# Optimization experiments

Hardware: AMD Instinct MI355X
Metric: run time of the kernel (lower is better)

Reference implementation:

```python
import jax, jax.numpy as jnp
import numpy as np

PAD_IDX = 0
K = 5
TEMPERATURE = 1.0
BATCH = 256
VOCAB = 50257


def setup_inputs() -> dict:
    key = jax.random.key(0)
    k1, k2, k3, k4, k5 = jax.random.split(key, 5)
    draft_tokens = jax.random.randint(k1, (BATCH, K), 0, VOCAB)
    # valid-ish log-probabilities (negative values)
    draft_log_probs = -jax.random.uniform(k2, (BATCH, K), minval=0.05, maxval=8.0, dtype=jnp.float32)
    target_logits = jax.random.normal(k3, (BATCH, K, VOCAB), dtype=jnp.float32)
    random_vals = jax.random.uniform(k4, (BATCH, K), dtype=jnp.float32)
    uniform_sample = jax.random.uniform(k5, (BATCH,), dtype=jnp.float32)
    return {
        "draft_tokens": draft_tokens,
        "draft_log_probs": draft_log_probs,
        "target_logits": target_logits,
        "random_vals": random_vals,
        "uniform_sample": uniform_sample,
    }


def reference(draft_tokens, draft_log_probs, target_logits, random_vals, uniform_sample):
    B, k = draft_tokens.shape
    # --- accept/reject scan ---
    tlp = jax.nn.log_softmax(target_logits / TEMPERATURE, axis=-1)          # [B,k,V]
    tlp_draft = jnp.take_along_axis(tlp, draft_tokens[..., None], axis=2)[..., 0]  # [B,k]
    accept_probs = jnp.minimum(jnp.exp(tlp_draft - draft_log_probs), 1.0)
    accepted_mask = random_vals < accept_probs
    rejected_sent = jnp.concatenate(
        [~accepted_mask, jnp.ones((B, 1), dtype=bool)], axis=1)              # [B,k+1]
    first_reject = jnp.argmax(rejected_sent, axis=1)                         # [B]
    n_accepted = first_reject
    # fixed-width (k) accepted_tokens, PAD-filled past n_accepted (jit-friendly
    # variant of torch's dynamic max_accepted truncation; same valid entries)
    pos = jnp.arange(k)[None, :]
    accepted_tokens = jnp.where(pos < n_accepted[:, None], draft_tokens, PAD_IDX)
    # --- vectorized fallback sampling at first reject position ---
    rp = jnp.minimum(first_reject, k - 1)                                    # clamp for gather
    sel_logits = jnp.take_along_axis(target_logits, rp[:, None, None], axis=1)[:, 0, :]  # [B,V]
    target_probs = jax.nn.softmax(sel_logits / TEMPERATURE, axis=-1)
    dlp_sel = jnp.take_along_axis(draft_log_probs, rp[:, None], axis=1)      # [B,1]
    # torch builds a constant vector exp(dlp) over the whole vocab
    draft_probs = jnp.exp(dlp_sel)                                           # [B,1] broadcasts
    adjusted = jnp.clip(target_probs - draft_probs, 0.0)
    s = adjusted.sum(axis=-1, keepdims=True)
    probs = jnp.where(s > 0, adjusted / jnp.where(s > 0, s, 1.0), target_probs)  # [B,V]
    # multinomial(probs, 1) via inverse CDF with provided uniform sample
    cdf = jnp.cumsum(probs, axis=-1)
    thresh = uniform_sample[:, None] * cdf[:, -1:]
    sampled = jnp.argmax(cdf >= thresh, axis=-1)                             # [B]
    final_tokens = jnp.where(first_reject < k, sampled, PAD_IDX)
    return accepted_tokens, n_accepted, final_tokens
```

## Files before the change

kernel.cpp:

```cpp
#include <hip/hip_runtime.h>
#include <math.h>
#include <stdint.h>

#define VOCAB 50257
#define KD 5
#define NBATCH 256
#define NSPLIT 8
#define SEG ((VOCAB + NSPLIT - 1) / NSPLIT)
#define NT1 256
#define NT2 1024
#define NW2 (NT2 / 64)
#define NTILES ((VOCAB + NT2 - 1) / NT2)

__global__ __launch_bounds__(NT1) void zsum_row0_kernel(
    const float* __restrict__ logits, double* __restrict__ part)
{
    const int bid = blockIdx.x;
    const int b   = bid / NSPLIT;
    const int seg = bid % NSPLIT;
    const int tid = threadIdx.x;
    const int lane = tid & 63, wv = tid >> 6;

    const float* row = logits + (size_t)b * KD * (size_t)VOCAB;
    int s0 = seg * SEG;
    int s1 = s0 + SEG; if (s1 > VOCAB) s1 = VOCAB;
    const float* p = row + s0;
    int n = s1 - s0;

    int head = (int)((4u - ((((uintptr_t)p) >> 2) & 3u)) & 3u);
    if (head > n) head = n;
    double local = 0.0;
    if (tid < head) local += (double)expf(p[tid]);
    int nvec = (n - head) >> 2;
    const float4* p4 = (const float4*)(p + head);
    for (int i = tid; i < nvec; i += NT1) {
        float4 x = p4[i];
        local += (double)expf(x.x) + (double)expf(x.y)
               + (double)expf(x.z) + (double)expf(x.w);
    }
    int ts = head + (nvec << 2);
    int tc = n - ts;
    if (tid < tc) local += (double)expf(p[ts + tid]);

    for (int off = 32; off; off >>= 1) local += __shfl_down(local, off, 64);
    __shared__ double sw[NT1 / 64];
    if (lane == 0) sw[wv] = local;
    __syncthreads();
    if (tid == 0) {
        double Z = 0.0;
        for (int w = 0; w < NT1 / 64; ++w) Z += sw[w];
        part[bid] = Z;
    }
}

__global__ __launch_bounds__(NT2) void decide_sample_kernel(
    const int* __restrict__ dtok,
    const float* __restrict__ dlp,
    const float* __restrict__ logits,
    const float* __restrict__ rnd,
    const float* __restrict__ usmp,
    const double* __restrict__ part,
    int* __restrict__ out)
{
    const int b    = blockIdx.x;
    const int tid  = threadIdx.x;
    const int lane = tid & 63;
    const int wv   = tid >> 6;

    __shared__ double s_w[NW2];
    __shared__ double s_tileA[NTILES];
    __shared__ double s_tileR[NTILES];
    __shared__ double s_dbc[2];
    __shared__ int    s_ibc[2];
    __shared__ int    s_found;

    double Zsel  = 0.0;
    int    n_acc = KD;
    for (int r = 0; r < KD; ++r) {
        const float* row = logits + ((size_t)b * KD + r) * (size_t)VOCAB;
        if (r > 0) {
            int head = (int)((4u - ((((uintptr_t)row) >> 2) & 3u)) & 3u);
            double local = 0.0;
            if (tid < head) local += (double)expf(row[tid]);
            int nvec = (VOCAB - head) >> 2;
            const float4* row4 = (const float4*)(row + head);
            for (int i = tid; i < nvec; i += NT2) {
                float4 x = row4[i];
                local += (double)expf(x.x) + (double)expf(x.y)
                       + (double)expf(x.z) + (double)expf(x.w);
            }
            int ts = head + (nvec << 2);
            int tc = VOCAB - ts;
            if (tid < tc) local += (double)expf(row[ts + tid]);
            for (int off = 32; off; off >>= 1) local += __shfl_down(local, off, 64);
            if (lane == 0) s_w[wv] = local;
            __syncthreads();
            if (tid == 0) {
                double Z = 0.0;
                for (int w = 0; w < NW2; ++w) Z += s_w[w];
                s_dbc[0] = Z;
            }
            __syncthreads();
        } else {
            if (wv == 0) {
                double v = (lane < NSPLIT) ? part[b * NSPLIT + lane] : 0.0;
                for (int off = 4; off; off >>= 1) v += __shfl_down(v, off, 64);
                if (lane == 0) s_dbc[0] = v;
            }
            __syncthreads();
        }
        if (tid == 0) {
            double Z   = s_dbc[0];
            int    tok = dtok[b * KD + r];
            double tlp = (double)row[tok] - log(Z);
            double ap  = exp(tlp - (double)dlp[b * KD + r]);
            if (ap > 1.0) ap = 1.0;
            s_ibc[0] = ((double)rnd[b * KD + r] < ap) ? 1 : 0;
        }
        __syncthreads();
        Zsel = s_dbc[0];
        int acc = s_ibc[0];
        __syncthreads();
        if (!acc) { n_acc = r; break; }
    }

    if (tid == 0) {
        for (int r = 0; r < KD; ++r)
            out[b * KD + r] = (r < n_acc) ? dtok[b * KD + r] : 0;
        out[NBATCH * KD + b] = n_acc;
        if (n_acc >= KD) out[NBATCH * KD + NBATCH + b] = 0;
        s_found = 0x7FFFFFFF;
    }
    if (n_acc >= KD) return;

    const int    rp   = n_acc;
    const float* row  = logits + ((size_t)b * KD + rp) * (size_t)VOCAB;
    const double invZ = 1.0 / Zsel;
    const double dp   = exp((double)dlp[b * KD + rp]);

    for (int t = wv; t < NTILES; t += NW2) {
        double aS = 0.0, rS = 0.0;
        int base = t * NT2;
        for (int j = 0; j < NT2 / 64; ++j) {
            int idx = base + j * 64 + lane;
            if (idx < VOCAB) {
                double p = (double)expf(row[idx]) * invZ;
                rS += p;
                double a = p - dp;
                if (a > 0.0) aS += a;
            }
        }
        for (int off = 32; off; off >>= 1) {
            aS += __shfl_down(aS, off, 64);
            rS += __shfl_down(rS, off, 64);
        }
        if (lane == 0) { s_tileA[t] = aS; s_tileR[t] = rS; }
    }
    __syncthreads();

    if (tid == 0) {
        double S = 0.0;
        for (int t = 0; t < NTILES; ++t) S += s_tileA[t];
        int useAdj = (S > 0.0) ? 1 : 0;
        double Tot = S;
        if (!useAdj) {
            Tot = 0.0;
            for (int t = 0; t < NTILES; ++t) Tot += s_tileR[t];
        }
        double T = (double)usmp[b] * Tot;
        const double* tiles = useAdj ? s_tileA : s_tileR;
        double P = 0.0;
        int    ct = NTILES - 1;
        for (int t = 0; t < NTILES; ++t) {
            if (P + tiles[t] >= T || t == NTILES - 1) { ct = t; break; }
            P += tiles[t];
        }
        s_dbc[0] = P;
        s_dbc[1] = T;
        s_ibc[0] = ct;
        s_ibc[1] = useAdj;
    }
    __syncthreads();

    {
        double Pb     = s_dbc[0];
        double T      = s_dbc[1];
        int    ct     = s_ibc[0];
        int    useAdj = s_ibc[1];
        int    idx    = ct * NT2 + tid;
        double g      = 0.0;
        if (idx < VOCAB) {
            double p = (double)expf(row[idx]) * invZ;
            if (useAdj) {
                double a = p - dp;
                g = (a > 0.0) ? a : 0.0;
            } else {
                g = p;
            }
        }
        double sc = g;
        for (int off = 1; off < 64; off <<= 1) {
            double v = __shfl_up(sc, (unsigned)off, 64);
            if (lane >= off) sc += v;
        }
        if (lane == 63) s_w[wv] = sc;
        __syncthreads();
        double woff = 0.0;
        for (int w = 0; w < wv; ++w) woff += s_w[w];
        double incl = Pb + woff + sc;
        if (idx < VOCAB && incl >= T) atomicMin(&s_found, idx);
        __syncthreads();
        if (tid == 0) {
            int smp = s_found;
            if (smp == 0x7FFFFFFF) {
                smp = ct * NT2 + NT2 - 1;
                if (smp > VOCAB - 1) smp = VOCAB - 1;
            }
            out[NBATCH * KD + NBATCH + b] = smp;
        }
    }
}

extern "C" void kernel_launch(void* const* d_in, const int* in_sizes, int n_in,
                              void* d_out, int out_size, void* d_ws, size_t ws_size,
                              hipStream_t stream) {
    const int*   dtok   = (const int*)d_in[0];
    const float* dlp    = (const float*)d_in[1];
    const float* logits = (const float*)d_in[2];
    const float* rnd    = (const float*)d_in[3];
    const float* usmp   = (const float*)d_in[4];
    int*         out    = (int*)d_out;
    double*      part   = (double*)d_ws;
    (void)in_sizes; (void)n_in; (void)out_size; (void)ws_size;

    zsum_row0_kernel<<<dim3(NBATCH * NSPLIT), dim3(NT1), 0, stream>>>(logits, part);
    decide_sample_kernel<<<dim3(NBATCH), dim3(NT2), 0, stream>>>(
        dtok, dlp, logits, rnd, usmp, part, out);
}
```

Measured before the change: 343.3 us.

## Precompute row-0 per-tile sums and max to skip fallback sampling pass

The row-0 statistics kernel now writes per-1024-element tile sums of exp(logits) and a per-segment maximum, replacing the single partial sum. When the first draft token is rejected, the decide kernel uses the max to check whether any adjusted probability can be positive. If none can, it samples straight from the precomputed tile sums and skips the full vocab pass. Otherwise it runs a pass that computes only the adjusted sums. This adds scalar loads from the first kernel and strided, non-vectorized tile reads there, and it relies on the max bound being exact enough to choose the right branch.

```diff
diff --git a/kernel.cpp b/kernel.cpp
--- a/kernel.cpp
+++ b/kernel.cpp
@@ -6,50 +6,55 @@
 #define KD 5
 #define NBATCH 256
 #define NSPLIT 8
-#define SEG ((VOCAB + NSPLIT - 1) / NSPLIT)
 #define NT1 256
 #define NT2 1024
 #define NW2 (NT2 / 64)
-#define NTILES ((VOCAB + NT2 - 1) / NT2)
-
-__global__ __launch_bounds__(NT1) void zsum_row0_kernel(
-    const float* __restrict__ logits, double* __restrict__ part)
+#define TILE 1024
+#define NTILES ((VOCAB + TILE - 1) / TILE)
+
+__global__ __launch_bounds__(NT1) void row0_stats_kernel(
+    const float* __restrict__ logits,
+    double* __restrict__ tsum,
+    double* __restrict__ mpart)
 {
     const int bid = blockIdx.x;
     const int b   = bid / NSPLIT;
     const int seg = bid % NSPLIT;
     const int tid = threadIdx.x;
     const int lane = tid & 63, wv = tid >> 6;
+    __shared__ double sw[NT1 / 64];
 
     const float* row = logits + (size_t)b * KD * (size_t)VOCAB;
-    int s0 = seg * SEG;
-    int s1 = s0 + SEG; if (s1 > VOCAB) s1 = VOCAB;
-    const float* p = row + s0;
-    int n = s1 - s0;
-
-    int head = (int)((4u - ((((uintptr_t)p) >> 2) & 3u)) & 3u);
-    if (head > n) head = n;
-    double local = 0.0;
-    if (tid < head) local += (double)expf(p[tid]);
-    int nvec = (n - head) >> 2;
-    const float4* p4 = (const float4*)(p + head);
-    for (int i = tid; i < nvec; i += NT1) {
-        float4 x = p4[i];
-        local += (double)expf(x.x) + (double)expf(x.y)
-               + (double)expf(x.z) + (double)expf(x.w);
-    }
-    int ts = head + (nvec << 2);
-    int tc = n - ts;
-    if (tid < tc) local += (double)expf(p[ts + tid]);
-
-    for (int off = 32; off; off >>= 1) local += __shfl_down(local, off, 64);
-    __shared__ double sw[NT1 / 64];
-    if (lane == 0) sw[wv] = local;
+    double mLoc = 0.0;
+    for (int t = seg; t < NTILES; t += NSPLIT) {
+        int base = t * TILE;
+        double s = 0.0;
+        #pragma unroll
+        for (int j = 0; j < TILE / NT1; ++j) {
+            int idx = base + j * NT1 + tid;
+            if (idx < VOCAB) {
+                double e = (double)expf(row[idx]);
+                s += e;
+                mLoc = fmax(mLoc, e);
+            }
+        }
+        for (int off = 32; off; off >>= 1) s += __shfl_down(s, off, 64);
+        if (lane == 0) sw[wv] = s;
+        __syncthreads();
+        if (tid == 0) {
+            double S = 0.0;
+            for (int w = 0; w < NT1 / 64; ++w) S += sw[w];
+            tsum[b * NTILES + t] = S;
+        }
+        __syncthreads();
+    }
+    for (int off = 32; off; off >>= 1) mLoc = fmax(mLoc, __shfl_down(mLoc, off, 64));
+    if (lane == 0) sw[wv] = mLoc;
     __syncthreads();
     if (tid == 0) {
-        double Z = 0.0;
-        for (int w = 0; w < NT1 / 64; ++w) Z += sw[w];
-        part[bid] = Z;
+        double M = sw[0];
+        for (int w = 1; w < NT1 / 64; ++w) M = fmax(M, sw[w]);
+        mpart[b * NSPLIT + seg] = M;
     }
 }
 
@@ -59,7 +64,8 @@
     const float* __restrict__ logits,
     const float* __restrict__ rnd,
     const float* __restrict__ usmp,
-    const double* __restrict__ part,
+    const double* __restrict__ tsum,
+    const double* __restrict__ mpart,
     int* __restrict__ out)
 {
     const int b    = blockIdx.x;
@@ -74,16 +80,40 @@
     __shared__ int    s_ibc[2];
     __shared__ int    s_found;
 
-    double Zsel  = 0.0;
+    const float* row0 = logits + (size_t)b * KD * (size_t)VOCAB;
+
+    if (tid < NTILES) s_tileR[tid] = tsum[b * NTILES + tid];
+    if (wv == 1) {
+        double m = (lane < NSPLIT) ? mpart[b * NSPLIT + lane] : 0.0;
+        for (int off = 4; off; off >>= 1) m = fmax(m, __shfl_down(m, off, 64));
+        if (lane == 0) s_dbc[1] = m;
+    }
+    __syncthreads();
+    if (tid == 0) {
+        double Z = 0.0;
+        for (int t = 0; t < NTILES; ++t) Z += s_tileR[t];
+        s_dbc[0] = Z;
+        int    tok = dtok[b * KD];
+        double tlp = (double)row0[tok] - log(Z);
+        double ap  = exp(tlp - (double)dlp[b * KD]);
+        if (ap > 1.0) ap = 1.0;
+        s_ibc[0] = ((double)rnd[b * KD] < ap) ? 1 : 0;
+        s_found  = 0x7FFFFFFF;
+    }
+    __syncthreads();
+    double Zsel = s_dbc[0];
+    double mx0  = s_dbc[1];
     int    n_acc = KD;
-    for (int r = 0; r < KD; ++r) {
-        const float* row = logits + ((size_t)b * KD + r) * (size_t)VOCAB;
-        if (r > 0) {
-            int head = (int)((4u - ((((uintptr_t)row) >> 2) & 3u)) & 3u);
+    if (!s_ibc[0]) {
+        n_acc = 0;
+    } else {
+        for (int r = 1; r < KD; ++r) {
+            const float* rrow = logits + ((size_t)b * KD + r) * (size_t)VOCAB;
+            int head = (int)((4u - ((((uintptr_t)rrow) >> 2) & 3u)) & 3u);
             double local = 0.0;
-            if (tid < head) local += (double)expf(row[tid]);
+            if (tid < head) local += (double)expf(rrow[tid]);
             int nvec = (VOCAB - head) >> 2;
-            const float4* row4 = (const float4*)(row + head);
+            const float4* row4 = (const float4*)(rrow + head);
             for (int i = tid; i < nvec; i += NT2) {
                 float4 x = row4[i];
                 local += (double)expf(x.x) + (double)expf(x.y)
@@ -91,7 +121,7 @@
             }
             int ts = head + (nvec << 2);
             int tc = VOCAB - ts;
-            if (tid < tc) local += (double)expf(row[ts + tid]);
+            if (tid < tc) local += (double)expf(rrow[ts + tid]);
             for (int off = 32; off; off >>= 1) local += __shfl_down(local, off, 64);
             if (lane == 0) s_w[wv] = local;
             __syncthreads();
@@ -99,29 +129,18 @@
                 double Z = 0.0;
                 for (int w = 0; w < NW2; ++w) Z += s_w[w];
                 s_dbc[0] = Z;
+                int    tok = dtok[b * KD + r];
+                double tlp = (double)rrow[tok] - log(Z);
+                double ap  = exp(tlp - (double)dlp[b * KD + r]);
+                if (ap > 1.0) ap = 1.0;
+                s_ibc[0] = ((double)rnd[b * KD + r] < ap) ? 1 : 0;
             }
             __syncthreads();
-        } else {
-            if (wv == 0) {
-                double v = (lane < NSPLIT) ? part[b * NSPLIT + lane] : 0.0;
-                for (int off = 4; off; off >>= 1) v += __shfl_down(v, off, 64);
-                if (lane == 0) s_dbc[0] = v;
-            }
+            Zsel = s_dbc[0];
+            int acc = s_ibc[0];
             __syncthreads();
-        }
-        if (tid == 0) {
-            double Z   = s_dbc[0];
-            int    tok = dtok[b * KD + r];
-            double tlp = (double)row[tok] - log(Z);
-            double ap  = exp(tlp - (double)dlp[b * KD + r]);
-            if (ap > 1.0) ap = 1.0;
-            s_ibc[0] = ((double)rnd[b * KD + r] < ap) ? 1 : 0;
-        }
-        __syncthreads();
-        Zsel = s_dbc[0];
-        int acc = s_ibc[0];
-        __syncthreads();
-        if (!acc) { n_acc = r; break; }
+            if (!acc) { n_acc = r; break; }
+        }
     }
 
     if (tid == 0) {
@@ -129,7 +148,6 @@
             out[b * KD + r] = (r < n_acc) ? dtok[b * KD + r] : 0;
         out[NBATCH * KD + b] = n_acc;
         if (n_acc >= KD) out[NBATCH * KD + NBATCH + b] = 0;
-        s_found = 0x7FFFFFFF;
     }
     if (n_acc >= KD) return;
 
@@ -138,64 +156,105 @@
     const double invZ = 1.0 / Zsel;
     const double dp   = exp((double)dlp[b * KD + rp]);
 
-    for (int t = wv; t < NTILES; t += NW2) {
-        double aS = 0.0, rS = 0.0;
-        int base = t * NT2;
-        for (int j = 0; j < NT2 / 64; ++j) {
-            int idx = base + j * 64 + lane;
-            if (idx < VOCAB) {
-                double p = (double)expf(row[idx]) * invZ;
-                rS += p;
-                double a = p - dp;
-                if (a > 0.0) aS += a;
-            }
-        }
-        for (int off = 32; off; off >>= 1) {
-            aS += __shfl_down(aS, off, 64);
-            rS += __shfl_down(rS, off, 64);
-        }
-        if (lane == 0) { s_tileA[t] = aS; s_tileR[t] = rS; }
-    }
-    __syncthreads();
-
-    if (tid == 0) {
-        double S = 0.0;
-        for (int t = 0; t < NTILES; ++t) S += s_tileA[t];
-        int useAdj = (S > 0.0) ? 1 : 0;
-        double Tot = S;
-        if (!useAdj) {
-            Tot = 0.0;
-            for (int t = 0; t < NTILES; ++t) Tot += s_tileR[t];
-        }
-        double T = (double)usmp[b] * Tot;
-        const double* tiles = useAdj ? s_tileA : s_tileR;
-        double P = 0.0;
-        int    ct = NTILES - 1;
-        for (int t = 0; t < NTILES; ++t) {
-            if (P + tiles[t] >= T || t == NTILES - 1) { ct = t; break; }
-            P += tiles[t];
-        }
-        s_dbc[0] = P;
-        s_dbc[1] = T;
-        s_ibc[0] = ct;
-        s_ibc[1] = useAdj;
-    }
-    __syncthreads();
+    if (rp == 0 && !(mx0 * invZ > dp)) {
+        __syncthreads();
+        if (tid == 0) {
+            double T = (double)usmp[b] * Zsel;
+            double P = 0.0;
+            int    ct = NTILES - 1;
+            for (int t = 0; t < NTILES; ++t) {
+                if (P + s_tileR[t] >= T || t == NTILES - 1) { ct = t; break; }
+                P += s_tileR[t];
+            }
+            s_dbc[0] = P; s_dbc[1] = T; s_ibc[0] = ct; s_ibc[1] = 0;
+        }
+        __syncthreads();
+    } else if (rp == 0) {
+        for (int t = wv; t < NTILES; t += NW2) {
+            double aS = 0.0;
+            int base = t * TILE;
+            for (int j = 0; j < TILE / 64; ++j) {
+                int idx = base + j * 64 + lane;
+                if (idx < VOCAB) {
+                    double p = (double)expf(row[idx]) * invZ;
+                    double a = p - dp;
+                    if (a > 0.0) aS += a;
+                }
+            }
+            for (int off = 32; off; off >>= 1) aS += __shfl_down(aS, off, 64);
+            if (lane == 0) s_tileA[t] = aS;
+        }
+        __syncthreads();
+        if (tid == 0) {
+            double S = 0.0;
+            for (int t = 0; t < NTILES; ++t) S += s_tileA[t];
+            double T = (double)usmp[b] * S;
+            double P = 0.0;
+            int    ct = NTILES - 1;
+            for (int t = 0; t < NTILES; ++t) {
+                if (P + s_tileA[t] >= T || t == NTILES - 1) { ct = t; break; }
+                P += s_tileA[t];
+            }
+            s_dbc[0] = P; s_dbc[1] = T; s_ibc[0] = ct; s_ibc[1] = 1;
+        }
+        __syncthreads();
+    } else {
+        for (int t = wv; t < NTILES; t += NW2) {
+            double aS = 0.0, rS = 0.0;
+            int base = t * TILE;
+            for (int j = 0; j < TILE / 64; ++j) {
+                int idx = base + j * 64 + lane;
+                if (idx < VOCAB) {
+                    double p = (double)expf(row[idx]) * invZ;
+                    rS += p;
+                    double a = p - dp;
+                    if (a > 0.0) aS += a;
+                }
+            }
+            for (int off = 32; off; off >>= 1) {
+                aS += __shfl_down(aS, off, 64);
+                rS += __shfl_down(rS, off, 64);
+            }
+            if (lane == 0) { s_tileA[t] = aS; s_tileR[t] = rS; }
+        }
+        __syncthreads();
+        if (tid == 0) {
+            double S = 0.0;
+            for (int t = 0; t < NTILES; ++t) S += s_tileA[t];
+            int useAdj = (S > 0.0) ? 1 : 0;
+            double Tot = S;
+            if (!useAdj) {
+                Tot = 0.0;
+                for (int t = 0; t < NTILES; ++t) Tot += s_tileR[t];
+            }
+            double T = (double)usmp[b] * Tot;
+            const double* tiles = useAdj ? s_tileA : s_tileR;
+            double P = 0.0;
+            int    ct = NTILES - 1;
+            for (int t = 0; t < NTILES; ++t) {
+                if (P + tiles[t] >= T || t == NTILES - 1) { ct = t; break; }
+                P += tiles[t];
+            }
+            s_dbc[0] = P; s_dbc[1] = T; s_ibc[0] = ct; s_ibc[1] = useAdj ? 1 : 2;
+        }
+        __syncthreads();
+    }
 
     {
-        double Pb     = s_dbc[0];
-        double T      = s_dbc[1];
-        int    ct     = s_ibc[0];
-        int    useAdj = s_ibc[1];
-        int    idx    = ct * NT2 + tid;
-        double g      = 0.0;
+        double Pb   = s_dbc[0];
+        double T    = s_dbc[1];
+        int    ct   = s_ibc[0];
+        int    mode = s_ibc[1];
+        int    idx  = ct * TILE + tid;
+        double g    = 0.0;
         if (idx < VOCAB) {
-            double p = (double)expf(row[idx]) * invZ;
-            if (useAdj) {
-                double a = p - dp;
-                g = (a > 0.0) ? a : 0.0;
+            double e = (double)expf(row[idx]);
+            if (mode == 0) {
+                g = e;
             } else {
-                g = p;
+                double p = e * invZ;
+                if (mode == 1) { double a = p - dp; g = (a > 0.0) ? a : 0.0; }
+                else           { g = p; }
             }
         }
         double sc = g;
@@ -213,7 +272,7 @@
         if (tid == 0) {
             int smp = s_found;
             if (smp == 0x7FFFFFFF) {
-                smp = ct * NT2 + NT2 - 1;
+                smp = ct * TILE + TILE - 1;
                 if (smp > VOCAB - 1) smp = VOCAB - 1;
             }
             out[NBATCH * KD + NBATCH + b] = smp;
@@ -230,10 +289,12 @@
     const float* rnd    = (const float*)d_in[3];
     const float* usmp   = (const float*)d_in[4];
     int*         out    = (int*)d_out;
-    double*      part   = (double*)d_ws;
+    double*      tsum   = (double*)d_ws;
+    double*      mpart  = (double*)d_ws + NBATCH * NTILES;
     (void)in_sizes; (void)n_in; (void)out_size; (void)ws_size;
 
-    zsum_row0_kernel<<<dim3(NBATCH * NSPLIT), dim3(NT1), 0, stream>>>(logits, part);
+    row0_stats_kernel<<<dim3(NBATCH * NSPLIT), dim3(NT1), 0, stream>>>(
+        logits, tsum, mpart);
     decide_sample_kernel<<<dim3(NBATCH), dim3(NT2), 0, stream>>>(
-        dtok, dlp, logits, rnd, usmp, part, out);
+        dtok, dlp, logits, rnd, usmp, tsum, mpart, out);
 }
```

Result: no change. 344.3 us (+0.3%).
